# Kernel tuning notes

Measured on AMD Instinct MI355X. Metric: run time of the kernel, lower is better.

## Reference

```python
import jax, jax.numpy as jnp
import numpy as np

EMB = 512
HEADS = 8
HEAD_DIM = EMB // HEADS
GN_EPS = 1e-6
THETA_SCALE = 10000.0


def _multiply_by_i(x):
    # interleave: out[..., 2i] = -x[..., 2i+1], out[..., 2i+1] = x[..., 2i]
    return jnp.stack((-x[..., 1::2], x[..., ::2]), axis=-1).reshape(x.shape)


def _theta_shift(x, sin, cos):
    return x * cos + _multiply_by_i(x) * sin


def setup_inputs() -> dict:
    key = jax.random.key(0)
    ks = jax.random.split(key, 13)
    B, N, E = 2, 2048, EMB

    def xavier(k, out_dim, in_dim):
        std = (2.0 / (out_dim + in_dim)) ** 0.5
        return std * jax.random.normal(k, (out_dim, in_dim), dtype=jnp.float32)

    return {
        "query": jax.random.normal(ks[0], (B, N, E), dtype=jnp.float32),
        "k": jax.random.normal(ks[1], (B, N, E), dtype=jnp.float32),
        "v": jax.random.normal(ks[2], (B, N, E), dtype=jnp.float32),
        "Wq": xavier(ks[3], E, E), "bq": jnp.zeros((E,), jnp.float32),
        "Wk": xavier(ks[4], E, E), "bk": jnp.zeros((E,), jnp.float32),
        "Wv": xavier(ks[5], E, E), "bv": jnp.zeros((E,), jnp.float32),
        "Wg": xavier(ks[6], E, E), "bg": jnp.zeros((E,), jnp.float32),
        "Wo": xavier(ks[7], E, E), "bo": jnp.zeros((E,), jnp.float32),
    }


def reference(query, k, v, Wq, bq, Wk, bk, Wv, bv, Wg, bg, Wo, bo):
    B, N, E = query.shape
    H, D = HEADS, E // HEADS

    def proj(x, W, b):  # torch Linear: x @ W.T + b, then split heads -> [b h n d]
        return (x @ W.T + b).reshape(B, N, H, D).transpose(0, 2, 1, 3)

    q = proj(query, Wq, bq)
    kk = proj(k, Wk, bk)
    vv = proj(v, Wv, bv)

    # rotary-style theta shift; thetas repeated pairwise [t0,t0,t1,t1,...]
    thetas = jnp.repeat(1.0 / THETA_SCALE ** jnp.linspace(0.0, 1.0, D // 2), 2)
    angles = jnp.arange(N, dtype=jnp.float32)[:, None] * thetas[None, :]  # [n d]
    sin = jnp.sin(angles)[None, None]
    cos = jnp.cos(angles)[None, None]
    q = _theta_shift(q, sin, cos)
    kk = _theta_shift(kk, sin, cos)

    # decay-masked retention (softmax-free)
    gammas = 1.0 - jnp.exp(jnp.linspace(np.log(1 / 32), np.log(1 / 512), H)).astype(jnp.float32)
    pos = jnp.arange(N)
    dist = jnp.abs(pos[:, None] - pos[None, :]).astype(jnp.float32)
    causal = pos[:, None] >= pos[None, :]
    decay_mask = jnp.where(causal[None], gammas[:, None, None] ** dist[None], 0.0)  # [h n s]

    kk = kk / (D ** 0.5)
    sim = jnp.einsum('bhnd,bhsd->bhns', q, kk) * decay_mask[None]  # [b h n n]
    ret = jnp.einsum('bhns,bhsd->bhnd', sim, vv)

    # GroupNorm(groups=H, channels=H, affine=False) over (b n) samples -> per-(b,h,n) norm over d
    mean = ret.mean(axis=-1, keepdims=True)
    var = ret.var(axis=-1, keepdims=True)
    ret = (ret - mean) / jnp.sqrt(var + GN_EPS)

    ret = ret.transpose(0, 2, 1, 3).reshape(B, N, E)
    gate = jax.nn.silu(query @ Wg.T + bg)
    out = (ret * gate) @ Wo.T + bo
    return out
```

## Files before the change

### kernel.cpp

```cpp
#include <hip/hip_runtime.h>
#include <math.h>

typedef float f32x4 __attribute__((ext_vector_type(4)));
typedef short s16x8 __attribute__((ext_vector_type(8)));
typedef short s16x4 __attribute__((ext_vector_type(4)));
typedef unsigned u32x4 __attribute__((ext_vector_type(4)));

__device__ __forceinline__ short f2bf(float f) {
    unsigned u = __builtin_bit_cast(unsigned, f);
    unsigned r = u + 0x7FFFu + ((u >> 16) & 1u);
    return (short)(r >> 16);
}
__device__ __forceinline__ float bf2f(short h) {
    return __builtin_bit_cast(float, ((unsigned)(unsigned short)h) << 16);
}
__device__ __forceinline__ unsigned pack2(short a, short b) {
    return (unsigned)(unsigned short)a | ((unsigned)(unsigned short)b << 16);
}
__device__ __forceinline__ unsigned cvtpk(float a, float b) {
    unsigned r;
    asm("v_cvt_pk_bf16_f32 %0, %1, %2" : "=v"(r) : "v"(a), "v"(b));
    return r;
}

__device__ __forceinline__ void split16v(const float* __restrict__ p,
                                         short* __restrict__ h,
                                         short* __restrict__ l) {
    f32x4 a0 = *(const f32x4*)(p);
    f32x4 a1 = *(const f32x4*)(p + 4);
    f32x4 a2 = *(const f32x4*)(p + 8);
    f32x4 a3 = *(const f32x4*)(p + 12);
    #pragma unroll
    for (int i = 0; i < 4; ++i) {
        short t0;
        t0 = f2bf(a0[i]); h[i]      = t0; l[i]      = f2bf(a0[i] - bf2f(t0));
        t0 = f2bf(a1[i]); h[4 + i]  = t0; l[4 + i]  = f2bf(a1[i] - bf2f(t0));
        t0 = f2bf(a2[i]); h[8 + i]  = t0; l[8 + i]  = f2bf(a2[i] - bf2f(t0));
        t0 = f2bf(a3[i]); h[12 + i] = t0; l[12 + i] = f2bf(a3[i] - bf2f(t0));
    }
}

__device__ __forceinline__ void gload16(const void* g, void* l) {
    __builtin_amdgcn_global_load_lds(
        (const __attribute__((address_space(1))) unsigned int*)g,
        (__attribute__((address_space(3))) unsigned int*)l,
        16, 0, 0);
}

__device__ __forceinline__ void decay_params(int h, int n0, float& l2g, int& stLo) {
    float lg0 = logf(1.0f / 32.0f), lg1 = logf(1.0f / 512.0f);
    float om = expf(lg0 + (float)h * (lg1 - lg0) * (1.0f / 7.0f));
    l2g = log2f(1.0f - om);
    int Dcut = (int)(11.5129255f / om) + 64;
    stLo = (n0 - Dcut) >> 6;
    if (stLo < 0) stLo = 0;
}

__global__ __launch_bounds__(256) void presplit_kernel(
    const float* __restrict__ W0, const float* __restrict__ W1,
    const float* __restrict__ W2, const float* __restrict__ W3,
    const float* __restrict__ W4,
    short* __restrict__ Wsp, float2* __restrict__ SC)
{
    const int blk = blockIdx.x;
    const int t = threadIdx.x;
    short hbuf[16], lbuf[16];
    if (blk < 256) {
        const int w = blk >> 6, bi = blk & 63;
        const float* src = (w == 0) ? W0 : (w == 1) ? W1 : (w == 2) ? W2 : W3;
        const int idx = (bi * 256 + t) * 16;
        const int row = idx >> 9, k0 = idx & 511;
        const int ntile = row >> 7, r = row & 127;
        const int kstep = k0 >> 5, kk0 = k0 & 31;
        const int s = (r & 3) << 4;
        split16v(src + idx, hbuf, lbuf);
        short* hp = Wsp + (long)w * 524288 + (ntile * 16 + kstep) * 8192 + r * 32;
        short* lp = hp + 4096;
        const int oA = ((2 * kk0) ^ s) >> 1;
        const int oB = ((2 * kk0 + 16) ^ s) >> 1;
        *(s16x8*)(hp + oA) = *(s16x8*)(hbuf);
        *(s16x8*)(hp + oB) = *(s16x8*)(hbuf + 8);
        *(s16x8*)(lp + oA) = *(s16x8*)(lbuf);
        *(s16x8*)(lp + oB) = *(s16x8*)(lbuf + 8);
    } else if (blk < 320) {
        const int bi = blk - 256;
        const int idx = (bi * 256 + t) * 16;
        short* hi = Wsp + (long)4 * 524288;
        short* lo = hi + 262144;
        split16v(W4 + idx, hbuf, lbuf);
        *(s16x8*)(hi + idx)     = *(s16x8*)(hbuf);
        *(s16x8*)(hi + idx + 8) = *(s16x8*)(hbuf + 8);
        *(s16x8*)(lo + idx)     = *(s16x8*)(lbuf);
        *(s16x8*)(lo + idx + 8) = *(s16x8*)(lbuf + 8);
    } else {
        const int gid = (blk - 320) * 256 + t;
        const int pos = gid >> 5, pp = gid & 31;
        const float theta = powf(10000.0f, -(float)pp * (1.0f / 31.0f));
        const float ang = (float)pos * theta;
        SC[gid] = make_float2(cosf(ang), sinf(ang));
    }
}

__global__ __launch_bounds__(512, 4) void projqkvg_kernel(
    const float* __restrict__ X0, const float* __restrict__ X1,
    const float* __restrict__ X2, const short* __restrict__ Wsp,
    const float* __restrict__ bq, const float* __restrict__ bk,
    const float* __restrict__ bv, const float* __restrict__ bg,
    const float2* __restrict__ SC,
    short* __restrict__ Qh, short* __restrict__ Ql,
    short* __restrict__ Kh, short* __restrict__ Vth,
    float* __restrict__ G)
{
    __shared__ __align__(16) short SB[36864];

    const int fid = blockIdx.x + 4 * (blockIdx.y + 64 * blockIdx.z);
    const int mtile = fid & 63;
    const int rr = fid >> 6;
    const int mode = rr & 3;
    const int ntile = rr >> 2;
    const int m0 = mtile * 64, n0 = ntile * 128;

    const int xi = (mode == 1) ? 1 : (mode == 2) ? 2 : 0;
    const float* Xf = (xi == 0) ? X0 : (xi == 1) ? X1 : X2;
    const float* bias = (mode == 0) ? bq : (mode == 1) ? bk
                       : (mode == 2) ? bv : bg;

    const int t = threadIdx.x, lane = t & 63, wv = t >> 6;
    const int wm = wv >> 2, wn = wv & 3;
    const int quad = lane >> 4, l15 = lane & 15;

    const short* Wblk = Wsp + (long)mode * 524288 + (long)ntile * 16 * 8192;

    const int c0 = wv * 3;
    const char* gs[3];
    int gstp[3];
    #pragma unroll
    for (int i = 0; i < 3; ++i) {
        const int c = c0 + i;
        if (c < 8) {
            const int u = c * 64 + lane;
            const int row = u >> 3, ucol = u & 7;
            gs[i] = (const char*)(Xf + (long)(m0 + row) * 512)
                    + ((ucol ^ (row & 7)) << 4);
            gstp[i] = 128;
        } else {
            gs[i] = (const char*)(Wblk + (c - 8) * 512 + lane * 8);
            gstp[i] = 16384;
        }
    }

    auto STAGE = [&](int stg, int ks) {
        char* dstb = (char*)SB + stg * 24576 + c0 * 1024;
        #pragma unroll
        for (int i = 0; i < 3; ++i)
            gload16(gs[i] + ks * gstp[i], dstb + i * 1024);
    };

    int aoff[2];
    #pragma unroll
    for (int s2 = 0; s2 < 2; ++s2) {
        const int row = wm * 32 + s2 * 16 + l15;
        aoff[s2] = row * 128 + ((quad * 32) ^ ((row & 7) << 4));
    }
    const int sxw = (l15 & 3) << 4;
    int boff[2];
    #pragma unroll
    for (int s2 = 0; s2 < 2; ++s2)
        boff[s2] = 8192 + (wn * 32 + s2 * 16 + l15) * 64 + ((quad * 16) ^ sxw);

    f32x4 acc[2][2];
    #pragma unroll
    for (int i = 0; i < 2; ++i)
        #pragma unroll
        for (int j = 0; j < 2; ++j)
            acc[i][j] = (f32x4){0.f, 0.f, 0.f, 0.f};

    STAGE(0, 0);
    STAGE(1, 1);
    asm volatile("s_waitcnt vmcnt(3)" ::: "memory");
    __builtin_amdgcn_s_barrier();

    int cur = 0;
    for (int ks = 0; ks < 16; ++ks) {
        if (ks < 14) {
            int fill = cur + 2; if (fill >= 3) fill -= 3;
            STAGE(fill, ks + 2);
        }
        __builtin_amdgcn_sched_barrier(0);

        const char* stg = (const char*)SB + cur * 24576;
        s16x8 ah[2], al[2], bh[2], bl[2];
        #pragma unroll
        for (int s2 = 0; s2 < 2; ++s2) {
            f32x4 x0 = *(const f32x4*)(stg + aoff[s2]);
            f32x4 x1 = *(const f32x4*)(stg + (aoff[s2] ^ 16));
            u32x4 hv, lv;
            #pragma unroll
            for (int j = 0; j < 2; ++j) {
                float a0 = x0[2 * j], b0 = x0[2 * j + 1];
                float a1 = x1[2 * j], b1 = x1[2 * j + 1];
                unsigned h0 = cvtpk(a0, b0);
                unsigned h1 = cvtpk(a1, b1);
                hv[j]     = h0;
                hv[2 + j] = h1;
                float fa0 = __builtin_bit_cast(float, h0 << 16);
                float fb0 = __builtin_bit_cast(float, h0 & 0xFFFF0000u);
                float fa1 = __builtin_bit_cast(float, h1 << 16);
                float fb1 = __builtin_bit_cast(float, h1 & 0xFFFF0000u);
                lv[j]     = cvtpk(a0 - fa0, b0 - fb0);
                lv[2 + j] = cvtpk(a1 - fa1, b1 - fb1);
            }
            ah[s2] = __builtin_bit_cast(s16x8, hv);
            al[s2] = __builtin_bit_cast(s16x8, lv);
        }
        #pragma unroll
        for (int s2 = 0; s2 < 2; ++s2) {
            bh[s2] = *(const s16x8*)(stg + boff[s2]);
            bl[s2] = *(const s16x8*)(stg + 8192 + boff[s2]);
        }
        __builtin_amdgcn_s_setprio(1);
        #pragma unroll
        for (int i = 0; i < 2; ++i)
            #pragma unroll
            for (int j = 0; j < 2; ++j) {
                acc[i][j] = __builtin_amdgcn_mfma_f32_16x16x32_bf16(ah[i], bh[j], acc[i][j], 0, 0, 0);
                acc[i][j] = __builtin_amdgcn_mfma_f32_16x16x32_bf16(al[i], bh[j], acc[i][j], 0, 0, 0);
                acc[i][j] = __builtin_amdgcn_mfma_f32_16x16x32_bf16(ah[i], bl[j], acc[i][j], 0, 0, 0);
            }
        __builtin_amdgcn_s_setprio(0);

        if (ks < 14)       asm volatile("s_waitcnt vmcnt(3)" ::: "memory");
        else if (ks == 14) asm volatile("s_waitcnt vmcnt(0)" ::: "memory");
        __builtin_amdgcn_sched_barrier(0);
        __builtin_amdgcn_s_barrier();

        cur += 1; if (cur >= 3) cur -= 3;
    }

    __syncthreads();

    const int bb = m0 >> 11, posb = m0 & 2047;

    if (mode == 0) {
        short* Thi = SB + wv * 1280;
        short* Tlo = Thi + 640;
        const int head = (n0 >> 6) + (wn >> 1);
        const int dbase = (wn & 1) * 32;
        #pragma unroll
        for (int ms = 0; ms < 2; ++ms) {
            #pragma unroll
            for (int ns = 0; ns < 2; ++ns) {
                const int col = n0 + wn * 32 + ns * 16 + l15;
                const float bvv = bias[col];
                const int pp = (col & 63) >> 1;
                #pragma unroll
                for (int r = 0; r < 4; ++r) {
                    const int m = m0 + wm * 32 + ms * 16 + quad * 4 + r;
                    const int pos = m & 2047;
                    float x = acc[ms][ns][r] + bvv;
                    float prt = __shfl_xor(x, 1);
                    float2 sc = SC[pos * 32 + pp];
                    float y0 = x * sc.x - prt * sc.y;
                    float y1 = prt * sc.x + x * sc.y;
                    if (!(l15 & 1)) {
                        short h0 = f2bf(y0), h1 = f2bf(y1);
                        short l0 = f2bf(y0 - bf2f(h0)), l1 = f2bf(y1 - bf2f(h1));
                        const int o = (quad * 4 + r) * 40 + ns * 16 + l15;
                        *(unsigned*)&Thi[o] = pack2(h0, h1);
                        *(unsigned*)&Tlo[o] = pack2(l0, l1);
                    }
                }
            }
            const int mrow = wm * 32 + ms * 16;
            const int row = lane >> 2, ch = (lane & 3) * 8;
            s16x8 vh = *(const s16x8*)&Thi[row * 40 + ch];
            s16x8 vl = *(const s16x8*)&Tlo[row * 40 + ch];
            const long o = ((long)(bb * 8 + head) * 2048 + posb + mrow + row) * 64 + dbase + ch;
            *(s16x8*)(Qh + o) = vh;
            *(s16x8*)(Ql + o) = vl;
        }
    } else if (mode == 1) {
        short* Thi = SB + wv * 640;
        const int head = (n0 >> 6) + (wn >> 1);
        const int dbase = (wn & 1) * 32;
        #pragma unroll
        for (int ms = 0; ms < 2; ++ms) {
            #pragma unroll
            for (int ns = 0; ns < 2; ++ns) {
                const int col = n0 + wn * 32 + ns * 16 + l15;
                const float bvv = bias[col];
                const int pp = (col & 63) >> 1;
                #pragma unroll
                for (int r = 0; r < 4; ++r) {
                    const int m = m0 + wm * 32 + ms * 16 + quad * 4 + r;
                    const int pos = m & 2047;
                    float x = acc[ms][ns][r] + bvv;
                    float prt = __shfl_xor(x, 1);
                    float2 sc = SC[pos * 32 + pp];
                    float y0 = (x * sc.x - prt * sc.y) * 0.125f;
                    float y1 = (prt * sc.x + x * sc.y) * 0.125f;
                    if (!(l15 & 1)) {
                        const int o = (quad * 4 + r) * 40 + ns * 16 + l15;
                        *(unsigned*)&Thi[o] = pack2(f2bf(y0), f2bf(y1));
                    }
                }
            }
            const int mrow = wm * 32 + ms * 16;
            const int row = lane >> 2, ch = (lane & 3) * 8;
            s16x8 vh = *(const s16x8*)&Thi[row * 40 + ch];
            const long o = ((long)(bb * 8 + head) * 2048 + posb + mrow + row) * 64 + dbase + ch;
            *(s16x8*)(Kh + o) = vh;
        }
    } else if (mode == 2) {
        short* T2 = SB;
        #pragma unroll
        for (int ns = 0; ns < 2; ++ns) {
            const int col = n0 + wn * 32 + ns * 16 + l15;
            const float bvv = bias[col];
            #pragma unroll
            for (int ms = 0; ms < 2; ++ms) {
                s16x4 pk;
                #pragma unroll
                for (int r = 0; r < 4; ++r)
                    pk[r] = f2bf(acc[ms][ns][r] + bvv);
                *(s16x4*)&T2[(wn * 32 + ns * 16 + l15) * 72
                             + wm * 32 + ms * 16 + quad * 4] = pk;
            }
        }
        __syncthreads();
        #pragma unroll
        for (int pass = 0; pass < 2; ++pass) {
            const int row = pass * 64 + (t >> 3);
            const int ch = (t & 7) * 8;
            s16x8 v = *(const s16x8*)&T2[row * 72 + ch];
            const int head = (n0 >> 6) + (row >> 6);
            const int d = row & 63;
            const long o = ((long)(bb * 8 + head) * 64 + d) * 2048 + posb + ch;
            *(s16x8*)(Vth + o) = v;
        }
    } else {
        #pragma unroll
        for (int ns = 0; ns < 2; ++ns) {
            const int col = n0 + wn * 32 + ns * 16 + l15;
            const float bvv = bias[col];
            #pragma unroll
            for (int ms = 0; ms < 2; ++ms)
                #pragma unroll
                for (int r = 0; r < 4; ++r) {
                    const int m = m0 + wm * 32 + ms * 16 + quad * 4 + r;
                    float x = acc[ms][ns][r] + bvv;
                    G[(long)m * 512 + col] = x / (1.0f + expf(-x));
                }
        }
    }
}

__global__ __launch_bounds__(256) void attn_chunk_kernel(
    const short* __restrict__ Qh_g, const short* __restrict__ Ql_g,
    const short* __restrict__ Kh_g, const short* __restrict__ Vth_g,
    float* __restrict__ Racc)
{
    __shared__ __align__(16) short KhS[2][4608], VhS[2][4608];
    __shared__ __align__(16) short PhS[4352];

    const int fid = blockIdx.x;
    const int bh = fid & 15;
    const int rest = fid >> 4;
    const int qt = rest & 31;
    const int c  = rest >> 5;
    const int h = bh & 7;
    const int n0 = qt * 64;

    float l2g;
    int stLo;
    decay_params(h, n0, l2g, stLo);
    const int st0 = stLo + c * 16;
    if (st0 > qt) return;
    const int stHi = min(st0 + 15, qt);

    const int t = threadIdx.x, lane = t & 63, wv = t >> 6;
    const int quad = lane >> 4, l15 = lane & 15;
    const long base = (long)bh * 2048 * 64;

    float gneg[16];
    #pragma unroll
    for (int i = 0; i < 16; ++i)
        gneg[i] = exp2f(-(float)((i >> 2) * 16 + (i & 3)) * l2g);

    const int srow = t >> 2;
    const int scol = (t & 3) * 16;
    const int n = n0 + wv * 16 + l15;

    s16x8 qh[2], ql[2];
    {
        const short* qp  = Qh_g + base + (long)(n0 + wv * 16 + l15) * 64 + quad * 8;
        const short* qp2 = Ql_g + base + (long)(n0 + wv * 16 + l15) * 64 + quad * 8;
        qh[0] = *(const s16x8*)qp;
        qh[1] = *(const s16x8*)(qp + 32);
        ql[0] = *(const s16x8*)qp2;
        ql[1] = *(const s16x8*)(qp2 + 32);
    }

    f32x4 racc[4];
    #pragma unroll
    for (int i = 0; i < 4; ++i) racc[i] = (f32x4){0.f, 0.f, 0.f, 0.f};

    s16x8 pk0, pk1, pv0, pv1;
    {
        const long ko = base + (long)(st0 * 64 + srow) * 64 + scol;
        pk0 = *(const s16x8*)(Kh_g + ko);
        pk1 = *(const s16x8*)(Kh_g + ko + 8);
        const long vo = base + (long)srow * 2048 + st0 * 64 + scol;
        pv0 = *(const s16x8*)(Vth_g + vo);
        pv1 = *(const s16x8*)(Vth_g + vo + 8);
    }
    *(s16x8*)&KhS[0][srow * 72 + scol]     = pk0;
    *(s16x8*)&KhS[0][srow * 72 + scol + 8] = pk1;
    *(s16x8*)&VhS[0][srow * 72 + scol]     = pv0;
    *(s16x8*)&VhS[0][srow * 72 + scol + 8] = pv1;
    __syncthreads();

    int cur = 0;
    for (int st = st0; st <= stHi; ++st, cur ^= 1) {
        if (st < stHi) {
            const long ko = base + (long)((st + 1) * 64 + srow) * 64 + scol;
            pk0 = *(const s16x8*)(Kh_g + ko);
            pk1 = *(const s16x8*)(Kh_g + ko + 8);
            const long vo = base + (long)srow * 2048 + (st + 1) * 64 + scol;
            pv0 = *(const s16x8*)(Vth_g + vo);
            pv1 = *(const s16x8*)(Vth_g + vo + 8);
        }

        const short* khs = KhS[cur];
        const short* vhs = VhS[cur];
        const int s0 = st * 64;
        const float t0 = exp2f((float)(n - s0 - quad * 4) * l2g);

        #pragma unroll
        for (int sub = 0; sub < 4; ++sub) {
            const int ro = (sub * 16 + l15) * 72 + quad * 8;
            s16x8 kh0 = *(const s16x8*)&khs[ro];
            s16x8 kh1 = *(const s16x8*)&khs[ro + 32];
            f32x4 sacc = (f32x4){0.f, 0.f, 0.f, 0.f};
            sacc = __builtin_amdgcn_mfma_f32_16x16x32_bf16(kh0, qh[0], sacc, 0, 0, 0);
            sacc = __builtin_amdgcn_mfma_f32_16x16x32_bf16(kh1, qh[1], sacc, 0, 0, 0);
            sacc = __builtin_amdgcn_mfma_f32_16x16x32_bf16(kh0, ql[0], sacc, 0, 0, 0);
            sacc = __builtin_amdgcn_mfma_f32_16x16x32_bf16(kh1, ql[1], sacc, 0, 0, 0);

            const int sb = s0 + sub * 16 + quad * 4;
            s16x4 pkh;
            #pragma unroll
            for (int r = 0; r < 4; ++r) {
                const int s = sb + r;
                const float wgt = (n >= s) ? t0 * gneg[sub * 4 + r] : 0.0f;
                pkh[r] = f2bf(sacc[r] * wgt);
            }
            *(s16x4*)&PhS[(wv * 16 + l15) * 68 + sub * 16 + quad * 4] = pkh;
        }

        const int pro = (wv * 16 + l15) * 68 + quad * 8;
        s16x8 ph0 = *(const s16x8*)&PhS[pro];
        s16x8 ph1 = *(const s16x8*)&PhS[pro + 32];
        #pragma unroll
        for (int ds = 0; ds < 4; ++ds) {
            const int ro = (ds * 16 + l15) * 72 + quad * 8;
            s16x8 vh0 = *(const s16x8*)&vhs[ro];
            s16x8 vh1 = *(const s16x8*)&vhs[ro + 32];
            racc[ds] = __builtin_amdgcn_mfma_f32_16x16x32_bf16(ph0, vh0, racc[ds], 0, 0, 0);
            racc[ds] = __builtin_amdgcn_mfma_f32_16x16x32_bf16(ph1, vh1, racc[ds], 0, 0, 0);
        }

        if (st < stHi) {
            short* kd = KhS[cur ^ 1];
            short* vd = VhS[cur ^ 1];
            *(s16x8*)&kd[srow * 72 + scol]     = pk0;
            *(s16x8*)&kd[srow * 72 + scol + 8] = pk1;
            *(s16x8*)&vd[srow * 72 + scol]     = pv0;
            *(s16x8*)&vd[srow * 72 + scol + 8] = pv1;
        }
        __syncthreads();
    }

    float* dst = Racc + (long)((bh * 32 + qt) * 2 + c) * 4096;
    #pragma unroll
    for (int ds = 0; ds < 4; ++ds)
        #pragma unroll
        for (int r = 0; r < 4; ++r)
            dst[(wv * 16 + quad * 4 + r) * 64 + ds * 16 + l15] = racc[ds][r];
}

__global__ __launch_bounds__(256) void attn_finish_kernel(
    const float* __restrict__ Racc, const float* __restrict__ G,
    short* __restrict__ RGh)
{
    __shared__ __align__(16) short rgS[4608];

    const int fid = blockIdx.x;
    const int bh = fid & 15;
    const int qt = fid >> 4;
    const int h = bh & 7, b = bh >> 3;
    const int n0 = qt * 64;

    float l2g;
    int stLo;
    decay_params(h, n0, l2g, stLo);
    const int ntiles = qt - stLo + 1;
    const int nc = (ntiles + 15) >> 4;

    const int t = threadIdx.x, lane = t & 63, wv = t >> 6;
    const int quad = lane >> 4, l15 = lane & 15;

    const float* s0 = Racc + (long)((bh * 32 + qt) * 2) * 4096;
    f32x4 racc[4];
    #pragma unroll
    for (int ds = 0; ds < 4; ++ds)
        #pragma unroll
        for (int r = 0; r < 4; ++r) {
            const int o = (wv * 16 + quad * 4 + r) * 64 + ds * 16 + l15;
            float v = s0[o];
            if (nc > 1) v += s0[4096 + o];
            racc[ds][r] = v;
        }

    float mean[4], rstd[4];
    #pragma unroll
    for (int r = 0; r < 4; ++r) {
        float s = racc[0][r] + racc[1][r] + racc[2][r] + racc[3][r];
        s += __shfl_xor(s, 1); s += __shfl_xor(s, 2);
        s += __shfl_xor(s, 4); s += __shfl_xor(s, 8);
        mean[r] = s * (1.0f / 64.0f);
        float vs = 0.f;
        #pragma unroll
        for (int ds = 0; ds < 4; ++ds) {
            float d = racc[ds][r] - mean[r];
            vs += d * d;
        }
        vs += __shfl_xor(vs, 1); vs += __shfl_xor(vs, 2);
        vs += __shfl_xor(vs, 4); vs += __shfl_xor(vs, 8);
        rstd[r] = rsqrtf(vs * (1.0f / 64.0f) + 1e-6f);
    }

    short* rgH = rgS + wv * 1152;
    #pragma unroll
    for (int ds = 0; ds < 4; ++ds) {
        #pragma unroll
        for (int r = 0; r < 4; ++r) {
            const int nn = n0 + wv * 16 + quad * 4 + r;
            const int d = ds * 16 + l15;
            const long gi = ((long)(b * 2048 + nn)) * 512 + h * 64 + d;
            float rg = (racc[ds][r] - mean[r]) * rstd[r] * G[gi];
            float prt = __shfl_xor(rg, 1);
            if (!(l15 & 1)) {
                const int o = (quad * 4 + r) * 72 + ds * 16 + l15;
                *(unsigned*)&rgH[o] = pack2(f2bf(rg), f2bf(prt));
            }
        }
    }
    __syncthreads();
    #pragma unroll
    for (int p2 = 0; p2 < 2; ++p2) {
        const int row = p2 * 8 + (lane >> 3);
        const int ch = (lane & 7) * 8;
        s16x8 vh = *(const s16x8*)&rgH[row * 72 + ch];
        const int nn = n0 + wv * 16 + row;
        const long o = ((long)(b * 2048 + nn)) * 512 + h * 64 + ch;
        *(s16x8*)(RGh + o) = vh;
    }
}

__global__ __launch_bounds__(256) void projo_kernel(
    const short* __restrict__ RGh, const short* __restrict__ Woh_g,
    const float* __restrict__ bo, float* __restrict__ out)
{
    __shared__ __align__(16) char PB[46080];

    const short* Wol_g = Woh_g + 262144;
    const int t = threadIdx.x, lane = t & 63, wv = t >> 6;
    const int wm = wv >> 1, wn = wv & 1;
    const int quad = lane >> 4, l15 = lane & 15;
    const int m0 = blockIdx.y * 32, n0 = blockIdx.x * 128;

    f32x4 acc[4];
    #pragma unroll
    for (int j = 0; j < 4; ++j) acc[j] = (f32x4){0.f, 0.f, 0.f, 0.f};

    const int xrow = t >> 3, xcol = (t & 7) * 4;
    const int wrow = t >> 1, wcol = (t & 1) * 16;
    const long xbase = (long)(m0 + xrow) * 512 + xcol;
    const long wbase = (long)(n0 + wrow) * 512 + wcol;

    s16x4 px;
    s16x8 pw0, pw1, pw2, pw3;
    px  = *(const s16x4*)(RGh + xbase);
    pw0 = *(const s16x8*)(Woh_g + wbase);
    pw1 = *(const s16x8*)(Woh_g + wbase + 8);
    pw2 = *(const s16x8*)(Wol_g + wbase);
    pw3 = *(const s16x8*)(Wol_g + wbase + 8);

    {
        short* XhS = (short*)PB;
        short* WhS = XhS + 1280;
        short* WlS = XhS + 6400;
        *(s16x4*)&XhS[xrow * 40 + xcol]     = px;
        *(s16x8*)&WhS[wrow * 40 + wcol]     = pw0;
        *(s16x8*)&WhS[wrow * 40 + wcol + 8] = pw1;
        *(s16x8*)&WlS[wrow * 40 + wcol]     = pw2;
        *(s16x8*)&WlS[wrow * 40 + wcol + 8] = pw3;
    }
    __syncthreads();

    for (int k0 = 0; k0 < 512; k0 += 32) {
        const int cur = (k0 >> 5) & 1;
        const bool more = (k0 + 32 < 512);
        if (more) {
            const long xo = xbase + k0 + 32;
            const long wo = wbase + k0 + 32;
            px  = *(const s16x4*)(RGh + xo);
            pw0 = *(const s16x8*)(Woh_g + wo);
            pw1 = *(const s16x8*)(Woh_g + wo + 8);
            pw2 = *(const s16x8*)(Wol_g + wo);
            pw3 = *(const s16x8*)(Wol_g + wo + 8);
        }

        const short* XhS = (const short*)(PB + cur * 23040);
        const short* WhS = XhS + 1280;
        const short* WlS = XhS + 6400;
        s16x8 ah, bh[4], bl[4];
        {
            const int ro = (wm * 16 + l15) * 40 + quad * 8;
            ah = *(const s16x8*)&XhS[ro];
        }
        #pragma unroll
        for (int s = 0; s < 4; ++s) {
            const int ro = (wn * 64 + s * 16 + l15) * 40 + quad * 8;
            bh[s] = *(const s16x8*)&WhS[ro];
            bl[s] = *(const s16x8*)&WlS[ro];
        }
        #pragma unroll
        for (int j = 0; j < 4; ++j) {
            acc[j] = __builtin_amdgcn_mfma_f32_16x16x32_bf16(ah, bh[j], acc[j], 0, 0, 0);
            acc[j] = __builtin_amdgcn_mfma_f32_16x16x32_bf16(ah, bl[j], acc[j], 0, 0, 0);
        }

        if (more) {
            short* XhD = (short*)(PB + (cur ^ 1) * 23040);
            short* WhD = XhD + 1280;
            short* WlD = XhD + 6400;
            *(s16x4*)&XhD[xrow * 40 + xcol]     = px;
            *(s16x8*)&WhD[wrow * 40 + wcol]     = pw0;
            *(s16x8*)&WhD[wrow * 40 + wcol + 8] = pw1;
            *(s16x8*)&WlD[wrow * 40 + wcol]     = pw2;
            *(s16x8*)&WlD[wrow * 40 + wcol + 8] = pw3;
        }
        __syncthreads();
    }

    float* T = (float*)PB + wv * 1152;
    #pragma unroll
    for (int ns = 0; ns < 4; ++ns) {
        const int col = n0 + wn * 64 + ns * 16 + l15;
        const float bvv = bo[col];
        #pragma unroll
        for (int r = 0; r < 4; ++r)
            T[(quad * 4 + r) * 72 + ns * 16 + l15] = acc[ns][r] + bvv;
    }
    #pragma unroll
    for (int it = 0; it < 2; ++it) {
        const int row = it * 8 + (lane >> 3);
        const int ch = (lane & 7) * 8;
        f32x4 a = *(const f32x4*)&T[row * 72 + ch];
        f32x4 c = *(const f32x4*)&T[row * 72 + ch + 4];
        const long o = (long)(m0 + wm * 16 + row) * 512 + n0 + wn * 64 + ch;
        *(f32x4*)(out + o) = a;
        *(f32x4*)(out + o + 4) = c;
    }
}

extern "C" void kernel_launch(void* const* d_in, const int* in_sizes, int n_in,
                              void* d_out, int out_size, void* d_ws, size_t ws_size,
                              hipStream_t stream) {
    const float* query = (const float*)d_in[0];
    const float* kin   = (const float*)d_in[1];
    const float* vin   = (const float*)d_in[2];
    const float* Wq = (const float*)d_in[3];
    const float* bq = (const float*)d_in[4];
    const float* Wk = (const float*)d_in[5];
    const float* bk = (const float*)d_in[6];
    const float* Wv = (const float*)d_in[7];
    const float* bv = (const float*)d_in[8];
    const float* Wg = (const float*)d_in[9];
    const float* bg = (const float*)d_in[10];
    const float* Wo = (const float*)d_in[11];
    const float* bo = (const float*)d_in[12];

    short* S = (short*)d_ws;
    const long NE = 2097152;
    short* WSp = S;
    short* Xsp = S + 2621440;
    short* Qh  = Xsp + 12582912;
    short* Ql  = Qh + NE;
    short* Kh  = Ql + NE;
    short* Vth = Kh + NE;
    float* G   = (float*)(Vth + NE);
    short* RGh = (short*)(G + NE);
    float2* SC = (float2*)(RGh + NE);
    float* Racc = (float*)Xsp;

    presplit_kernel<<<576, 256, 0, stream>>>(
        Wq, Wk, Wv, Wg, Wo, WSp, SC);
    projqkvg_kernel<<<dim3(4, 64, 4), 512, 0, stream>>>(
        query, kin, vin, WSp, bq, bk, bv, bg, SC, Qh, Ql, Kh, Vth, G);
    attn_chunk_kernel<<<1024, 256, 0, stream>>>(
        Qh, Ql, Kh, Vth, Racc);
    attn_finish_kernel<<<512, 256, 0, stream>>>(
        Racc, G, RGh);
    projo_kernel<<<dim3(4, 128), 256, 0, stream>>>(
        RGh, WSp + 4 * 524288, bo, (float*)d_out);
}
```

Measured before the change: 190.0 us.

## Fuse groupnorm-gate into single-chunk attention blocks; load X directly in projection

The attention chunk kernel now finishes query tiles whose decay window fits in one chunk itself. It applies the group norm and the gate multiply and writes the bf16 RGh output directly, so those tiles skip the Racc round trip and attn_finish exits early for them. Separately, the QKVG projection no longer stages the fp32 activation tile through LDS. Each lane loads X straight from global memory into registers, which cuts LDS use and raises occupancy, but the X loads are now exposed global latency inside the K loop.

```diff
diff --git a/kernel.cpp b/kernel.cpp
--- a/kernel.cpp
+++ b/kernel.cpp
@@ -111,7 +111,7 @@
     short* __restrict__ Kh, short* __restrict__ Vth,
     float* __restrict__ G)
 {
-    __shared__ __align__(16) short SB[36864];
+    __shared__ __align__(16) short SB[24576];
 
     const int fid = blockIdx.x + 4 * (blockIdx.y + 64 * blockIdx.z);
     const int mtile = fid & 63;
@@ -131,42 +131,29 @@
 
     const short* Wblk = Wsp + (long)mode * 524288 + (long)ntile * 16 * 8192;
 
-    const int c0 = wv * 3;
-    const char* gs[3];
-    int gstp[3];
-    #pragma unroll
-    for (int i = 0; i < 3; ++i) {
-        const int c = c0 + i;
-        if (c < 8) {
-            const int u = c * 64 + lane;
-            const int row = u >> 3, ucol = u & 7;
-            gs[i] = (const char*)(Xf + (long)(m0 + row) * 512)
-                    + ((ucol ^ (row & 7)) << 4);
-            gstp[i] = 128;
-        } else {
-            gs[i] = (const char*)(Wblk + (c - 8) * 512 + lane * 8);
-            gstp[i] = 16384;
-        }
-    }
+    const int c0 = wv * 2;
+    const char* gs[2];
+    #pragma unroll
+    for (int i = 0; i < 2; ++i)
+        gs[i] = (const char*)(Wblk + (c0 + i) * 512 + lane * 8);
 
     auto STAGE = [&](int stg, int ks) {
-        char* dstb = (char*)SB + stg * 24576 + c0 * 1024;
-        #pragma unroll
-        for (int i = 0; i < 3; ++i)
-            gload16(gs[i] + ks * gstp[i], dstb + i * 1024);
+        char* dstb = (char*)SB + stg * 16384 + c0 * 1024;
+        #pragma unroll
+        for (int i = 0; i < 2; ++i)
+            gload16(gs[i] + (long)ks * 16384, dstb + i * 1024);
     };
 
-    int aoff[2];
-    #pragma unroll
-    for (int s2 = 0; s2 < 2; ++s2) {
-        const int row = wm * 32 + s2 * 16 + l15;
-        aoff[s2] = row * 128 + ((quad * 32) ^ ((row & 7) << 4));
-    }
+    const float* xp[2];
+    #pragma unroll
+    for (int s2 = 0; s2 < 2; ++s2)
+        xp[s2] = Xf + (long)(m0 + wm * 32 + s2 * 16 + l15) * 512 + quad * 8;
+
     const int sxw = (l15 & 3) << 4;
     int boff[2];
     #pragma unroll
     for (int s2 = 0; s2 < 2; ++s2)
-        boff[s2] = 8192 + (wn * 32 + s2 * 16 + l15) * 64 + ((quad * 16) ^ sxw);
+        boff[s2] = (wn * 32 + s2 * 16 + l15) * 64 + ((quad * 16) ^ sxw);
 
     f32x4 acc[2][2];
     #pragma unroll
@@ -177,28 +164,32 @@
 
     STAGE(0, 0);
     STAGE(1, 1);
-    asm volatile("s_waitcnt vmcnt(3)" ::: "memory");
+    asm volatile("s_waitcnt vmcnt(2)" ::: "memory");
     __builtin_amdgcn_s_barrier();
 
     int cur = 0;
     for (int ks = 0; ks < 16; ++ks) {
+        f32x4 x0[2], x1[2];
+        #pragma unroll
+        for (int s2 = 0; s2 < 2; ++s2) {
+            x0[s2] = *(const f32x4*)(xp[s2] + ks * 32);
+            x1[s2] = *(const f32x4*)(xp[s2] + ks * 32 + 4);
+        }
         if (ks < 14) {
             int fill = cur + 2; if (fill >= 3) fill -= 3;
             STAGE(fill, ks + 2);
         }
         __builtin_amdgcn_sched_barrier(0);
 
-        const char* stg = (const char*)SB + cur * 24576;
+        const char* stg = (const char*)SB + cur * 16384;
         s16x8 ah[2], al[2], bh[2], bl[2];
         #pragma unroll
         for (int s2 = 0; s2 < 2; ++s2) {
-            f32x4 x0 = *(const f32x4*)(stg + aoff[s2]);
-            f32x4 x1 = *(const f32x4*)(stg + (aoff[s2] ^ 16));
             u32x4 hv, lv;
             #pragma unroll
             for (int j = 0; j < 2; ++j) {
-                float a0 = x0[2 * j], b0 = x0[2 * j + 1];
-                float a1 = x1[2 * j], b1 = x1[2 * j + 1];
+                float a0 = x0[s2][2 * j], b0 = x0[s2][2 * j + 1];
+                float a1 = x1[s2][2 * j], b1 = x1[s2][2 * j + 1];
                 unsigned h0 = cvtpk(a0, b0);
                 unsigned h1 = cvtpk(a1, b1);
                 hv[j]     = h0;
@@ -229,7 +220,7 @@
             }
         __builtin_amdgcn_s_setprio(0);
 
-        if (ks < 14)       asm volatile("s_waitcnt vmcnt(3)" ::: "memory");
+        if (ks < 14)       asm volatile("s_waitcnt vmcnt(2)" ::: "memory");
         else if (ks == 14) asm volatile("s_waitcnt vmcnt(0)" ::: "memory");
         __builtin_amdgcn_sched_barrier(0);
         __builtin_amdgcn_s_barrier();
@@ -358,6 +349,7 @@
 __global__ __launch_bounds__(256) void attn_chunk_kernel(
     const short* __restrict__ Qh_g, const short* __restrict__ Ql_g,
     const short* __restrict__ Kh_g, const short* __restrict__ Vth_g,
+    const float* __restrict__ G, short* __restrict__ RGh,
     float* __restrict__ Racc)
 {
     __shared__ __align__(16) short KhS[2][4608], VhS[2][4608];
@@ -368,12 +360,13 @@
     const int rest = fid >> 4;
     const int qt = rest & 31;
     const int c  = rest >> 5;
-    const int h = bh & 7;
+    const int h = bh & 7, b = bh >> 3;
     const int n0 = qt * 64;
 
     float l2g;
     int stLo;
     decay_params(h, n0, l2g, stLo);
+    const int ntiles = qt - stLo + 1;
     const int st0 = stLo + c * 16;
     if (st0 > qt) return;
     const int stHi = min(st0 + 15, qt);
@@ -481,6 +474,52 @@
         __syncthreads();
     }
 
+    if (c == 0 && ntiles <= 16) {
+        float mean[4], rstd[4];
+        #pragma unroll
+        for (int r = 0; r < 4; ++r) {
+            float s = racc[0][r] + racc[1][r] + racc[2][r] + racc[3][r];
+            s += __shfl_xor(s, 1); s += __shfl_xor(s, 2);
+            s += __shfl_xor(s, 4); s += __shfl_xor(s, 8);
+            mean[r] = s * (1.0f / 64.0f);
+            float vs = 0.f;
+            #pragma unroll
+            for (int ds = 0; ds < 4; ++ds) {
+                float d = racc[ds][r] - mean[r];
+                vs += d * d;
+            }
+            vs += __shfl_xor(vs, 1); vs += __shfl_xor(vs, 2);
+            vs += __shfl_xor(vs, 4); vs += __shfl_xor(vs, 8);
+            rstd[r] = rsqrtf(vs * (1.0f / 64.0f) + 1e-6f);
+        }
+        short* rgH = (short*)KhS + wv * 1152;
+        #pragma unroll
+        for (int ds = 0; ds < 4; ++ds) {
+            #pragma unroll
+            for (int r = 0; r < 4; ++r) {
+                const int nn = n0 + wv * 16 + quad * 4 + r;
+                const int d = ds * 16 + l15;
+                const long gi = ((long)(b * 2048 + nn)) * 512 + h * 64 + d;
+                float rg = (racc[ds][r] - mean[r]) * rstd[r] * G[gi];
+                float prt = __shfl_xor(rg, 1);
+                if (!(l15 & 1)) {
+                    const int o = (quad * 4 + r) * 72 + ds * 16 + l15;
+                    *(unsigned*)&rgH[o] = pack2(f2bf(rg), f2bf(prt));
+                }
+            }
+        }
+        #pragma unroll
+        for (int p2 = 0; p2 < 2; ++p2) {
+            const int row = p2 * 8 + (lane >> 3);
+            const int ch = (lane & 7) * 8;
+            s16x8 vh = *(const s16x8*)&rgH[row * 72 + ch];
+            const int nn = n0 + wv * 16 + row;
+            const long o = ((long)(b * 2048 + nn)) * 512 + h * 64 + ch;
+            *(s16x8*)(RGh + o) = vh;
+        }
+        return;
+    }
+
     float* dst = Racc + (long)((bh * 32 + qt) * 2 + c) * 4096;
     #pragma unroll
     for (int ds = 0; ds < 4; ++ds)
@@ -505,7 +544,7 @@
     int stLo;
     decay_params(h, n0, l2g, stLo);
     const int ntiles = qt - stLo + 1;
-    const int nc = (ntiles + 15) >> 4;
+    if (ntiles <= 16) return;
 
     const int t = threadIdx.x, lane = t & 63, wv = t >> 6;
     const int quad = lane >> 4, l15 = lane & 15;
@@ -517,9 +556,7 @@
         #pragma unroll
         for (int r = 0; r < 4; ++r) {
             const int o = (wv * 16 + quad * 4 + r) * 64 + ds * 16 + l15;
-            float v = s0[o];
-            if (nc > 1) v += s0[4096 + o];
-            racc[ds][r] = v;
+            racc[ds][r] = s0[o] + s0[4096 + o];
         }
 
     float mean[4], rstd[4];
@@ -711,7 +748,7 @@
     projqkvg_kernel<<<dim3(4, 64, 4), 512, 0, stream>>>(
         query, kin, vin, WSp, bq, bk, bv, bg, SC, Qh, Ql, Kh, Vth, G);
     attn_chunk_kernel<<<1024, 256, 0, stream>>>(
-        Qh, Ql, Kh, Vth, Racc);
+        Qh, Ql, Kh, Vth, G, RGh, Racc);
     attn_finish_kernel<<<512, 256, 0, stream>>>(
         Racc, G, RGh);
     projo_kernel<<<dim3(4, 128), 256, 0, stream>>>(
```

New measurement: 230.6 us. 21.3% more time.
